# Kernel tuning notes

Measured on AMD Instinct MI355X. Metric: run time of the kernel, lower is better.

Reference implementation:

```python
import jax, jax.numpy as jnp
import numpy as np

B, N, DIM = 4, 4096, 1024
HEADS, DIM_HEAD = 16, 64
DIM_INNER = HEADS * DIM_HEAD
ATTN_SCALE = 8.0
EPS = 1e-12  # F.normalize default eps


def setup_inputs() -> dict:
    key = jax.random.key(0)
    k1, k2, k3, k4, k5 = jax.random.split(key, 5)
    x = jax.random.normal(k1, (B, N, DIM), dtype=jnp.float32)
    gamma = jnp.ones((DIM,), dtype=jnp.float32)
    # stored as (in, out) so forward is x @ w
    w_qkv = jax.random.normal(k2, (DIM, 3 * DIM_INNER), dtype=jnp.float32) * (DIM ** -0.5)
    temperature = jnp.ones((HEADS, 1, 1), dtype=jnp.float32)
    w_out = jax.random.normal(k3, (DIM_INNER, DIM), dtype=jnp.float32) * (DIM_INNER ** -0.5)
    return {"x": x, "gamma": gamma, "w_qkv": w_qkv, "temperature": temperature, "w_out": w_out}


def _l2norm(t):
    # F.normalize(t, dim=-1): t / max(||t||_2, eps)
    n = jnp.linalg.norm(t, axis=-1, keepdims=True)
    return t / jnp.maximum(n, EPS)


def reference(x, gamma, w_qkv, temperature, w_out):
    b, n, dim = x.shape
    # RMSNorm: F.normalize(x, dim=-1) * sqrt(dim) * gamma
    xn = _l2norm(x) * (dim ** 0.5) * gamma
    # QKV projection -> qkv b h d n
    qkv = (xn @ w_qkv).reshape(b, n, 3, HEADS, DIM_HEAD)
    qkv = qkv.transpose(2, 0, 3, 4, 1)  # (3, b, h, d, n)
    q, k, v = qkv[0], qkv[1], qkv[2]
    # l2-normalize q, k over the sequence (last) axis; temperature-scale q
    q = _l2norm(q) * jnp.exp(temperature)  # temperature: (h,1,1) broadcast
    k = _l2norm(k)
    # cross-covariance attention over the small channel dim d
    sim = jnp.einsum('bhdn,bhen->bhde', q, k) * ATTN_SCALE
    attn = jax.nn.softmax(sim, axis=-1)
    out = jnp.einsum('bhde,bhen->bhdn', attn, v)
    # b h d n -> b n (h d), then out projection
    out = out.transpose(0, 3, 1, 2).reshape(b, n, DIM_INNER)
    return out @ w_out
```

## Files before the change

kernel.cpp:

```cpp
#include <hip/hip_runtime.h>
#include <stdint.h>

typedef unsigned short u16;
typedef unsigned int u32;
typedef __attribute__((ext_vector_type(8))) __bf16 bf16x8;
typedef __attribute__((ext_vector_type(4))) float f32x4;

#define M_TOT 16384
#define DIMX  1024

__device__ __forceinline__ u16 f2b(float f) {
  u32 u = __builtin_bit_cast(u32, f);
  u32 r = (u + 0x7fffu + ((u >> 16) & 1u)) >> 16;
  return (u16)r;
}

__device__ __forceinline__ void gl2lds16(const void* g, void* l) {
  __builtin_amdgcn_global_load_lds((const __attribute__((address_space(1))) void*)g,
                                   (__attribute__((address_space(3))) void*)l,
                                   16, 0, 0);
}

__global__ __launch_bounds__(256) void k_rms(const float* __restrict__ x,
                                             const float* __restrict__ gamma,
                                             u16* __restrict__ xn) {
  int row = blockIdx.x;
  int t = threadIdx.x;
  const float4* xr = (const float4*)(x + (size_t)row * DIMX);
  float4 v = xr[t];
  float ss = v.x * v.x + v.y * v.y + v.z * v.z + v.w * v.w;
#pragma unroll
  for (int o = 32; o > 0; o >>= 1) ss += __shfl_xor(ss, o, 64);
  __shared__ float wss[4];
  int w = t >> 6;
  if ((t & 63) == 0) wss[w] = ss;
  __syncthreads();
  float tot = wss[0] + wss[1] + wss[2] + wss[3];
  float scale = 32.0f / fmaxf(sqrtf(tot), 1e-12f);
  float4 g = ((const float4*)gamma)[t];
  ushort4 o4;
  o4.x = f2b(v.x * scale * g.x);
  o4.y = f2b(v.y * scale * g.y);
  o4.z = f2b(v.z * scale * g.z);
  o4.w = f2b(v.w * scale * g.w);
  ((ushort4*)xn)[(size_t)row * 256 + t] = o4;
}

__global__ __launch_bounds__(256) void k_castT2(const float* __restrict__ wqkv,
                                                const float* __restrict__ wout,
                                                u16* __restrict__ wqT,
                                                u16* __restrict__ woT) {
  __shared__ float tile[32][33];
  const float* in; u16* out; int Cc; int c0;
  if (blockIdx.x < 96) { in = wqkv; out = wqT; Cc = 3072; c0 = blockIdx.x * 32; }
  else                 { in = wout; out = woT; Cc = 1024; c0 = (blockIdx.x - 96) * 32; }
  int r0 = blockIdx.y * 32;
  int tx = threadIdx.x, ty = threadIdx.y;
#pragma unroll
  for (int i = 0; i < 4; i++)
    tile[ty + i * 8][tx] = in[(size_t)(r0 + ty + i * 8) * Cc + c0 + tx];
  __syncthreads();
#pragma unroll
  for (int i = 0; i < 4; i++)
    out[(size_t)(c0 + ty + i * 8) * 1024 + r0 + tx] = f2b(tile[tx][ty + i * 8]);
}


template<bool SWAP>
__device__ __forceinline__ f32x4 mf(bf16x8 a, bf16x8 b, f32x4 c) {
  return SWAP ? __builtin_amdgcn_mfma_f32_16x16x32_bf16(b, a, c, 0, 0, 0)
              : __builtin_amdgcn_mfma_f32_16x16x32_bf16(a, b, c, 0, 0, 0);
}

__device__ __forceinline__ void stage_ab(const u16* __restrict__ Ag,
                                         const u16* __restrict__ Bg,
                                         u16* dstA, u16* dstB, int t, int k0) {
#pragma unroll
  for (int r = 0; r < 2; r++) {
    int c = r * 512 + t;
    int row = c >> 2, s = c & 3;
    int g = s ^ ((row >> 1) & 3);
    gl2lds16(Ag + (size_t)row * 1024 + k0 + g * 8,
             dstA + (r * 512 + (t >> 6) * 64) * 8);
  }
  {
    int row = t >> 2, s = t & 3;
    int g = s ^ ((row >> 1) & 3);
    gl2lds16(Bg + (size_t)row * 1024 + k0 + g * 8,
             dstB + ((t >> 6) * 64) * 8);
  }
}

template<bool SWAP>
__device__ __forceinline__ void gemm_core(const u16* __restrict__ Ag,
                                          const u16* __restrict__ Bg,
                                          u16* lds, int t, f32x4 (&acc)[4][4]) {
  const int lane = t & 63;
  const int r16 = lane & 15, q = lane >> 4;
  const int wr = (t >> 6) >> 1, wc = (t >> 6) & 1;
  const int arow = wr * 64 + r16;
  const int brow = wc * 64 + r16;

  stage_ab(Ag, Bg, lds, lds + 8192, t, 0);
  asm volatile("s_waitcnt vmcnt(0)" ::: "memory");
  __builtin_amdgcn_s_barrier();

  bf16x8 af[4], bf[4];
#pragma unroll 1
  for (int tt = 0; tt < 32; tt++) {
    const int cur = (tt & 1) ? 12288 : 0;
    const int nxt = cur ^ 12288;
    const int k1 = ((tt + 1) & 31) << 5;
    stage_ab(Ag, Bg, lds + nxt, lds + nxt + 8192, t, k1);
    const u16* A = lds + cur;
    const u16* B = lds + cur + 8192;
#pragma unroll
    for (int i = 0; i < 4; i++) {
      int ar = i * 16 + arow;
      int br = i * 16 + brow;
      af[i] = *(const bf16x8*)(A + ar * 32 + (q ^ ((ar >> 1) & 3)) * 8);
      bf[i] = *(const bf16x8*)(B + br * 32 + (q ^ ((br >> 1) & 3)) * 8);
    }
    __builtin_amdgcn_s_setprio(1);
#pragma unroll
    for (int i = 0; i < 4; i++)
#pragma unroll
      for (int j = 0; j < 4; j++)
        acc[i][j] = mf<SWAP>(af[i], bf[j], acc[i][j]);
    __builtin_amdgcn_s_setprio(0);
    asm volatile("s_waitcnt vmcnt(0)" ::: "memory");
    __builtin_amdgcn_s_barrier();
  }
}

__global__ __launch_bounds__(512, 4) void k_gemm1(const u16* __restrict__ A,
                                                  const u16* __restrict__ Bt,
                                                  u16* __restrict__ qkT,
                                                  u16* __restrict__ vmat,
                                                  float* __restrict__ sumsq) {
  __shared__ u16 lds[2 * 12288];
  int l = blockIdx.x;
  int xcd = l & 7, c = l >> 3;
  int mt = xcd * 8 + (c & 7);
  int nt = c >> 3;
  int m0 = mt * 256, n0 = nt * 128;
  int t = threadIdx.x, lane = t & 63;
  int r16 = lane & 15, q = lane >> 4;
  int wr = (t >> 6) >> 1, wc = (t >> 6) & 1;
  f32x4 acc[4][4] = {};
  if (n0 < 2048) {
    gemm_core<false>(A + (size_t)m0 * 1024, Bt + (size_t)n0 * 1024, lds, t, acc);
    int b = m0 >> 12;
#pragma unroll
    for (int j = 0; j < 4; j++) {
      int cc = n0 + wc * 64 + j * 16 + r16;
      float colss = 0.f;
#pragma unroll
      for (int i = 0; i < 4; i++) {
        f32x4 a = acc[i][j];
        colss += a.x * a.x + a.y * a.y + a.z * a.z + a.w * a.w;
        int m = m0 + wr * 64 + i * 16 + q * 4;
        ushort4 o4;
        o4.x = f2b(a.x); o4.y = f2b(a.y); o4.z = f2b(a.z); o4.w = f2b(a.w);
        *(ushort4*)(qkT + (size_t)cc * M_TOT + m) = o4;
      }
      colss += __shfl_xor(colss, 16, 64);
      colss += __shfl_xor(colss, 32, 64);
      if (lane < 16) atomicAdd(&sumsq[b * 2048 + cc], colss);
    }
  } else {
    gemm_core<true>(A + (size_t)m0 * 1024, Bt + (size_t)n0 * 1024, lds, t, acc);
    int vc0 = n0 - 2048;
#pragma unroll
    for (int i = 0; i < 4; i++) {
      int m = m0 + wr * 64 + i * 16 + r16;
#pragma unroll
      for (int j = 0; j < 4; j++) {
        int cc = vc0 + wc * 64 + j * 16 + q * 4;
        f32x4 a = acc[i][j];
        ushort4 o4;
        o4.x = f2b(a.x); o4.y = f2b(a.y); o4.z = f2b(a.z); o4.w = f2b(a.w);
        *(ushort4*)(vmat + (size_t)m * 1024 + cc) = o4;
      }
    }
  }
}

__global__ __launch_bounds__(256) void k_attn_s(const u16* __restrict__ qkT,
                                                float* __restrict__ Spart) {
  __shared__ u16 Ql[64 * 256];
  __shared__ u16 Kl[64 * 256];
  int bh = blockIdx.x, split = blockIdx.y;
  int b = bh >> 4, h = bh & 15;
  int t = threadIdx.x, lane = t & 63, w = t >> 6;
  int r16 = lane & 15, q = lane >> 4;
  const u16* qbase = qkT + (size_t)(h * 64) * M_TOT + b * 4096 + split * 1024;
  const u16* kbase = qkT + (size_t)(1024 + h * 64) * M_TOT + b * 4096 + split * 1024;
  int drow = w * 16 + r16;
  f32x4 acc[4] = {};
#pragma unroll 1
  for (int it = 0; it < 4; it++) {
    int ncol = it * 256;
#pragma unroll
    for (int r = 0; r < 8; r++) {
      int ch = r * 256 + t;
      int row = ch >> 5;
      int sl = (ch & 31) ^ (row & 31);
      gl2lds16(qbase + (size_t)row * M_TOT + ncol + sl * 8,
               Ql + (r * 256 + w * 64) * 8);
      gl2lds16(kbase + (size_t)row * M_TOT + ncol + sl * 8,
               Kl + (r * 256 + w * 64) * 8);
    }
    asm volatile("s_waitcnt vmcnt(0)" ::: "memory");
    __syncthreads();
#pragma unroll
    for (int it2 = 0; it2 < 8; it2++) {
      bf16x8 aq = *(const bf16x8*)(Ql + drow * 256 + (((it2 * 4 + q) ^ (drow & 31)) * 8));
#pragma unroll
      for (int j = 0; j < 4; j++) {
        int erow = j * 16 + r16;
        bf16x8 bk = *(const bf16x8*)(Kl + erow * 256 + (((it2 * 4 + q) ^ (erow & 31)) * 8));
        acc[j] = __builtin_amdgcn_mfma_f32_16x16x32_bf16(bk, aq, acc[j], 0, 0, 0);
      }
    }
    __syncthreads();
  }
  float* Sp = Spart + ((size_t)split * 64 + bh) * 4096;
#pragma unroll
  for (int j = 0; j < 4; j++)
    *(f32x4*)(Sp + drow * 64 + j * 16 + q * 4) = acc[j];
}

__global__ __launch_bounds__(256) void k_softmax(const float* __restrict__ Spart,
                                                 const float* __restrict__ sumsq,
                                                 const float* __restrict__ temp,
                                                 u16* __restrict__ PT) {
  int bh = blockIdx.x;
  int b = bh >> 4, h = bh & 15;
  int t = threadIdx.x;
  int d = t & 63, w = t >> 6;
  int e0 = w * 16;
  __shared__ float rnk[64];
  __shared__ float redm[4][64];
  __shared__ float reds[4][64];
  if (t < 64) rnk[t] = 1.0f / fmaxf(sqrtf(sumsq[b * 2048 + 1024 + h * 64 + t]), 1e-12f);
  __syncthreads();
  float nq = sqrtf(sumsq[b * 2048 + h * 64 + d]);
  float qs = 8.0f * __expf(temp[h]) / fmaxf(nq, 1e-12f);
  const float* Sp = Spart + (size_t)bh * 4096 + d * 64 + e0;
  float vals[16];
#pragma unroll
  for (int e = 0; e < 16; e += 4) {
    f32x4 v = {};
#pragma unroll
    for (int s = 0; s < 4; s++)
      v += *(const f32x4*)(Sp + (size_t)s * 64 * 4096 + e);
    vals[e + 0] = v.x; vals[e + 1] = v.y; vals[e + 2] = v.z; vals[e + 3] = v.w;
  }
  float mx = -3.0e38f;
#pragma unroll
  for (int e = 0; e < 16; e++) {
    float v = vals[e] * qs * rnk[e0 + e];
    vals[e] = v;
    mx = fmaxf(mx, v);
  }
  redm[w][d] = mx;
  __syncthreads();
  float M = fmaxf(fmaxf(redm[0][d], redm[1][d]), fmaxf(redm[2][d], redm[3][d]));
  float s = 0.f;
#pragma unroll
  for (int e = 0; e < 16; e++) {
    float v = __expf(vals[e] - M);
    vals[e] = v;
    s += v;
  }
  reds[w][d] = s;
  __syncthreads();
  float inv = 1.0f / (reds[0][d] + reds[1][d] + reds[2][d] + reds[3][d]);
#pragma unroll
  for (int e = 0; e < 16; e++)
    PT[((size_t)bh * 64 + e0 + e) * 64 + d] = f2b(vals[e] * inv);
}

__global__ __launch_bounds__(256) void k_m(const u16* __restrict__ woT,
                                           const u16* __restrict__ PT,
                                           u16* __restrict__ MT) {
  int bh = blockIdx.x;
  int b = bh >> 4, h = bh & 15;
  int o0 = blockIdx.y * 128;
  int t = threadIdx.x, lane = t & 63, w = t >> 6;
  int r16 = lane & 15, q = lane >> 4;
  const u16* pbase = PT + (size_t)bh * 4096;
  f32x4 acc[2][4] = {};
#pragma unroll
  for (int ks = 0; ks < 2; ks++) {
    int kk = ks * 32 + q * 8;
    bf16x8 af[2], bfr[4];
#pragma unroll
    for (int i = 0; i < 2; i++)
      af[i] = *(const bf16x8*)(woT + (size_t)(o0 + w * 32 + i * 16 + r16) * 1024 + h * 64 + kk);
#pragma unroll
    for (int j = 0; j < 4; j++)
      bfr[j] = *(const bf16x8*)(pbase + (size_t)(j * 16 + r16) * 64 + kk);
#pragma unroll
    for (int i = 0; i < 2; i++)
#pragma unroll
      for (int j = 0; j < 4; j++)
        acc[i][j] = __builtin_amdgcn_mfma_f32_16x16x32_bf16(af[i], bfr[j], acc[i][j], 0, 0, 0);
  }
  u16* dst = MT + (size_t)b * 1024 * 1024;
#pragma unroll
  for (int i = 0; i < 2; i++) {
    int o = o0 + w * 32 + i * 16 + q * 4;
#pragma unroll
    for (int j = 0; j < 4; j++) {
      int e = h * 64 + j * 16 + r16;
      f32x4 a = acc[i][j];
      dst[(size_t)(o + 0) * 1024 + e] = f2b(a.x);
      dst[(size_t)(o + 1) * 1024 + e] = f2b(a.y);
      dst[(size_t)(o + 2) * 1024 + e] = f2b(a.z);
      dst[(size_t)(o + 3) * 1024 + e] = f2b(a.w);
    }
  }
}

__global__ __launch_bounds__(512, 4) void k_gemm2(const u16* __restrict__ A,
                                                  const u16* __restrict__ Bt,
                                                  float* __restrict__ C) {
  __shared__ u16 lds[2 * 12288];
  int l = blockIdx.x;
  int xcd = l & 7, c = l >> 3;
  int mt = xcd * 8 + (c & 7);
  int nt = c >> 3;
  int m0 = mt * 256, n0 = nt * 128;
  int b = m0 >> 12;
  const u16* Bb = Bt + (size_t)b * 1024 * 1024;
  int t = threadIdx.x, lane = t & 63;
  int r16 = lane & 15, q = lane >> 4;
  int wr = (t >> 6) >> 1, wc = (t >> 6) & 1;
  f32x4 acc[4][4] = {};
  gemm_core<true>(A + (size_t)m0 * 1024, Bb + (size_t)n0 * 1024, lds, t, acc);
#pragma unroll
  for (int i = 0; i < 4; i++) {
    int m = m0 + wr * 64 + i * 16 + r16;
#pragma unroll
    for (int j = 0; j < 4; j++) {
      int cc = n0 + wc * 64 + j * 16 + q * 4;
      *(f32x4*)(C + (size_t)m * 1024 + cc) = acc[i][j];
    }
  }
}

extern "C" void kernel_launch(void* const* d_in, const int* in_sizes, int n_in,
                              void* d_out, int out_size, void* d_ws, size_t ws_size,
                              hipStream_t stream) {
  const float* x     = (const float*)d_in[0];
  const float* gamma = (const float*)d_in[1];
  const float* wqkv  = (const float*)d_in[2];
  const float* temp  = (const float*)d_in[3];
  const float* wout  = (const float*)d_in[4];
  float* out = (float*)d_out;

  char* ws = (char*)d_ws;
  size_t off = 0;
  u16* xn = (u16*)(ws + off);    off += (size_t)M_TOT * 1024 * 2;
  u16* wqT = (u16*)(ws + off);   off += (size_t)3072 * 1024 * 2;
  u16* woT = (u16*)(ws + off);   off += (size_t)1024 * 1024 * 2;
  u16* qkT = (u16*)(ws + off);   off += (size_t)2048 * M_TOT * 2;
  u16* vmat = (u16*)(ws + off);  off += (size_t)M_TOT * 1024 * 2;
  float* sumsq = (float*)(ws + off); off += (size_t)4 * 2048 * 4;
  u16* PT = (u16*)(ws + off);    off += (size_t)64 * 64 * 64 * 2;
  u16* MT = (u16*)(ws + off);    off += (size_t)4 * 1024 * 1024 * 2;

  float* Spart = (float*)xn;

  hipMemsetAsync((void*)sumsq, 0, (size_t)4 * 2048 * 4, stream);

  k_rms<<<16384, 256, 0, stream>>>(x, gamma, xn);
  dim3 cb(32, 8);
  k_castT2<<<dim3(128, 32), cb, 0, stream>>>(wqkv, wout, wqT, woT);
  k_gemm1<<<1536, 512, 0, stream>>>(xn, wqT, qkT, vmat, sumsq);
  k_attn_s<<<dim3(64, 4), 256, 0, stream>>>(qkT, Spart);
  k_softmax<<<64, 256, 0, stream>>>(Spart, sumsq, temp, PT);
  k_m<<<dim3(64, 8), 256, 0, stream>>>(woT, PT, MT);
  k_gemm2<<<512, 512, 0, stream>>>(vmat, MT, out);
}
```

Baseline: 326.3 us.

## Reassociate attention via per-batch Gram matrix of normalized inputs

Computes the per-batch Gram matrix G = xn^T xn (1024x1024) once and derives the q·k similarities and the q/k column norms from W_q^T G W_k, so the full QKV projection over all tokens is no longer materialised. The value and output projections are folded into one per-batch matrix (W_v · attn-derived M), and the final output is a single GEMM of xn with it. This replaces the large 16384x3072 projection with smaller 1024-sized GEMMs, at the cost of an extra transpose of xn, a split-K partial buffer, and more bf16 rounding of intermediate products.

```diff
diff --git a/kernel.cpp b/kernel.cpp
--- a/kernel.cpp
+++ b/kernel.cpp
@@ -49,20 +49,48 @@
 __global__ __launch_bounds__(256) void k_castT2(const float* __restrict__ wqkv,
                                                 const float* __restrict__ wout,
                                                 u16* __restrict__ wqT,
-                                                u16* __restrict__ woT) {
+                                                u16* __restrict__ woT,
+                                                u16* __restrict__ wvc) {
   __shared__ float tile[32][33];
-  const float* in; u16* out; int Cc; int c0;
-  if (blockIdx.x < 96) { in = wqkv; out = wqT; Cc = 3072; c0 = blockIdx.x * 32; }
-  else                 { in = wout; out = woT; Cc = 1024; c0 = (blockIdx.x - 96) * 32; }
+  int bx = blockIdx.x;
   int r0 = blockIdx.y * 32;
   int tx = threadIdx.x, ty = threadIdx.y;
-#pragma unroll
-  for (int i = 0; i < 4; i++)
-    tile[ty + i * 8][tx] = in[(size_t)(r0 + ty + i * 8) * Cc + c0 + tx];
+  if (bx < 96) {
+    const float* in; u16* out; int Cc; int c0;
+    if (bx < 64) { in = wqkv; out = wqT; Cc = 3072; c0 = bx * 32; }
+    else         { in = wout; out = woT; Cc = 1024; c0 = (bx - 64) * 32; }
+#pragma unroll
+    for (int i = 0; i < 4; i++)
+      tile[ty + i * 8][tx] = in[(size_t)(r0 + ty + i * 8) * Cc + c0 + tx];
+    __syncthreads();
+#pragma unroll
+    for (int i = 0; i < 4; i++)
+      out[(size_t)(c0 + ty + i * 8) * 1024 + r0 + tx] = f2b(tile[tx][ty + i * 8]);
+  } else {
+    int c0 = (bx - 96) * 32;
+#pragma unroll
+    for (int i = 0; i < 4; i++) {
+      int r = r0 + ty + i * 8;
+      wvc[(size_t)r * 1024 + c0 + tx] = f2b(wqkv[(size_t)r * 3072 + 2048 + c0 + tx]);
+    }
+  }
+}
+
+__global__ __launch_bounds__(256) void k_xT(const u16* __restrict__ xn,
+                                            u16* __restrict__ xnT) {
+  __shared__ u16 tile[64][65];
+  int bz = blockIdx.z;
+  int n0 = blockIdx.x * 64, c0 = blockIdx.y * 64;
+  int tx = threadIdx.x, ty = threadIdx.y;
+  const u16* in = xn + (size_t)bz * 4096 * 1024;
+  u16* out = xnT + (size_t)bz * 1024 * 4096;
+#pragma unroll
+  for (int i = 0; i < 16; i++)
+    tile[ty + i * 4][tx] = in[(size_t)(n0 + ty + i * 4) * 1024 + c0 + tx];
   __syncthreads();
 #pragma unroll
-  for (int i = 0; i < 4; i++)
-    out[(size_t)(c0 + ty + i * 8) * 1024 + r0 + tx] = f2b(tile[tx][ty + i * 8]);
+  for (int i = 0; i < 16; i++)
+    out[(size_t)(c0 + ty + i * 4) * 4096 + n0 + tx] = tile[tx][ty + i * 4];
 }
 
 
@@ -74,19 +102,20 @@
 
 __device__ __forceinline__ void stage_ab(const u16* __restrict__ Ag,
                                          const u16* __restrict__ Bg,
-                                         u16* dstA, u16* dstB, int t, int k0) {
+                                         u16* dstA, u16* dstB, int t, int k0,
+                                         int ldA, int ldB) {
 #pragma unroll
   for (int r = 0; r < 2; r++) {
     int c = r * 512 + t;
     int row = c >> 2, s = c & 3;
     int g = s ^ ((row >> 1) & 3);
-    gl2lds16(Ag + (size_t)row * 1024 + k0 + g * 8,
+    gl2lds16(Ag + (size_t)row * ldA + k0 + g * 8,
              dstA + (r * 512 + (t >> 6) * 64) * 8);
   }
   {
     int row = t >> 2, s = t & 3;
     int g = s ^ ((row >> 1) & 3);
-    gl2lds16(Bg + (size_t)row * 1024 + k0 + g * 8,
+    gl2lds16(Bg + (size_t)row * ldB + k0 + g * 8,
              dstB + ((t >> 6) * 64) * 8);
   }
 }
@@ -94,24 +123,25 @@
 template<bool SWAP>
 __device__ __forceinline__ void gemm_core(const u16* __restrict__ Ag,
                                           const u16* __restrict__ Bg,
-                                          u16* lds, int t, f32x4 (&acc)[4][4]) {
+                                          u16* lds, int t, f32x4 (&acc)[4][4],
+                                          int ldA, int ldB, int nsteps) {
   const int lane = t & 63;
   const int r16 = lane & 15, q = lane >> 4;
   const int wr = (t >> 6) >> 1, wc = (t >> 6) & 1;
   const int arow = wr * 64 + r16;
   const int brow = wc * 64 + r16;
 
-  stage_ab(Ag, Bg, lds, lds + 8192, t, 0);
+  stage_ab(Ag, Bg, lds, lds + 8192, t, 0, ldA, ldB);
   asm volatile("s_waitcnt vmcnt(0)" ::: "memory");
   __builtin_amdgcn_s_barrier();
 
   bf16x8 af[4], bf[4];
 #pragma unroll 1
-  for (int tt = 0; tt < 32; tt++) {
+  for (int tt = 0; tt < nsteps; tt++) {
     const int cur = (tt & 1) ? 12288 : 0;
     const int nxt = cur ^ 12288;
-    const int k1 = ((tt + 1) & 31) << 5;
-    stage_ab(Ag, Bg, lds + nxt, lds + nxt + 8192, t, k1);
+    int k1 = (tt + 1 == nsteps) ? 0 : (tt + 1) * 32;
+    stage_ab(Ag, Bg, lds + nxt, lds + nxt + 8192, t, k1, ldA, ldB);
     const u16* A = lds + cur;
     const u16* B = lds + cur + 8192;
 #pragma unroll
@@ -133,106 +163,120 @@
   }
 }
 
-__global__ __launch_bounds__(512, 4) void k_gemm1(const u16* __restrict__ A,
-                                                  const u16* __restrict__ Bt,
-                                                  u16* __restrict__ qkT,
-                                                  u16* __restrict__ vmat,
-                                                  float* __restrict__ sumsq) {
+__global__ __launch_bounds__(512, 4) void k_G(const u16* __restrict__ xnT,
+                                              float* __restrict__ Gp) {
   __shared__ u16 lds[2 * 12288];
   int l = blockIdx.x;
-  int xcd = l & 7, c = l >> 3;
-  int mt = xcd * 8 + (c & 7);
-  int nt = c >> 3;
+  int s = l & 3, b = (l >> 2) & 3;
+  int tile = l >> 4;
+  int mt = tile >> 3, nt = tile & 7;
+  int m0 = mt * 256, n0 = nt * 128;
+  const u16* base = xnT + (size_t)b * 1024 * 4096 + s * 1024;
+  int t = threadIdx.x, lane = t & 63;
+  int r16 = lane & 15, q = lane >> 4;
+  int wr = (t >> 6) >> 1, wc = (t >> 6) & 1;
+  f32x4 acc[4][4] = {};
+  gemm_core<true>(base + (size_t)m0 * 4096, base + (size_t)n0 * 4096,
+                  lds, t, acc, 4096, 4096, 32);
+  float* C = Gp + (size_t)(s * 4 + b) * 1048576;
+#pragma unroll
+  for (int i = 0; i < 4; i++) {
+    int m = m0 + wr * 64 + i * 16 + r16;
+#pragma unroll
+    for (int j = 0; j < 4; j++) {
+      int cc = n0 + wc * 64 + j * 16 + q * 4;
+      *(f32x4*)(C + (size_t)m * 1024 + cc) = acc[i][j];
+    }
+  }
+}
+
+__global__ __launch_bounds__(256) void k_Gred(const float* __restrict__ Gp,
+                                              u16* __restrict__ G) {
+  size_t i = ((size_t)blockIdx.x * 256 + threadIdx.x) * 4;
+  f32x4 v = {};
+#pragma unroll
+  for (int s = 0; s < 4; s++)
+    v += *(const f32x4*)(Gp + (size_t)s * 4194304 + i);
+  ushort4 o4;
+  o4.x = f2b(v.x); o4.y = f2b(v.y); o4.z = f2b(v.z); o4.w = f2b(v.w);
+  *(ushort4*)(G + i) = o4;
+}
+
+__global__ __launch_bounds__(512, 4) void k_V(const u16* __restrict__ wqT,
+                                              const u16* __restrict__ G,
+                                              u16* __restrict__ V) {
+  __shared__ u16 lds[2 * 12288];
+  int l = blockIdx.x;
+  int b = l & 3;
+  int tile = l >> 2;
+  int mt = tile >> 3, nt = tile & 7;
   int m0 = mt * 256, n0 = nt * 128;
   int t = threadIdx.x, lane = t & 63;
   int r16 = lane & 15, q = lane >> 4;
   int wr = (t >> 6) >> 1, wc = (t >> 6) & 1;
   f32x4 acc[4][4] = {};
-  if (n0 < 2048) {
-    gemm_core<false>(A + (size_t)m0 * 1024, Bt + (size_t)n0 * 1024, lds, t, acc);
-    int b = m0 >> 12;
+  gemm_core<true>(wqT + (size_t)m0 * 1024,
+                  G + (size_t)b * 1048576 + (size_t)n0 * 1024,
+                  lds, t, acc, 1024, 1024, 32);
+  u16* out = V + (size_t)b * 2097152;
+#pragma unroll
+  for (int i = 0; i < 4; i++) {
+    int m = m0 + wr * 64 + i * 16 + r16;
 #pragma unroll
     for (int j = 0; j < 4; j++) {
-      int cc = n0 + wc * 64 + j * 16 + r16;
-      float colss = 0.f;
-#pragma unroll
-      for (int i = 0; i < 4; i++) {
-        f32x4 a = acc[i][j];
-        colss += a.x * a.x + a.y * a.y + a.z * a.z + a.w * a.w;
-        int m = m0 + wr * 64 + i * 16 + q * 4;
-        ushort4 o4;
-        o4.x = f2b(a.x); o4.y = f2b(a.y); o4.z = f2b(a.z); o4.w = f2b(a.w);
-        *(ushort4*)(qkT + (size_t)cc * M_TOT + m) = o4;
-      }
-      colss += __shfl_xor(colss, 16, 64);
-      colss += __shfl_xor(colss, 32, 64);
-      if (lane < 16) atomicAdd(&sumsq[b * 2048 + cc], colss);
-    }
-  } else {
-    gemm_core<true>(A + (size_t)m0 * 1024, Bt + (size_t)n0 * 1024, lds, t, acc);
-    int vc0 = n0 - 2048;
-#pragma unroll
-    for (int i = 0; i < 4; i++) {
-      int m = m0 + wr * 64 + i * 16 + r16;
-#pragma unroll
-      for (int j = 0; j < 4; j++) {
-        int cc = vc0 + wc * 64 + j * 16 + q * 4;
-        f32x4 a = acc[i][j];
-        ushort4 o4;
-        o4.x = f2b(a.x); o4.y = f2b(a.y); o4.z = f2b(a.z); o4.w = f2b(a.w);
-        *(ushort4*)(vmat + (size_t)m * 1024 + cc) = o4;
-      }
-    }
-  }
-}
-
-__global__ __launch_bounds__(256) void k_attn_s(const u16* __restrict__ qkT,
-                                                float* __restrict__ Spart) {
-  __shared__ u16 Ql[64 * 256];
-  __shared__ u16 Kl[64 * 256];
-  int bh = blockIdx.x, split = blockIdx.y;
+      int cc = n0 + wc * 64 + j * 16 + q * 4;
+      f32x4 a = acc[i][j];
+      ushort4 o4;
+      o4.x = f2b(a.x); o4.y = f2b(a.y); o4.z = f2b(a.z); o4.w = f2b(a.w);
+      *(ushort4*)(out + (size_t)m * 1024 + cc) = o4;
+    }
+  }
+}
+
+__global__ __launch_bounds__(256) void k_S(const u16* __restrict__ V,
+                                           const u16* __restrict__ wqT,
+                                           float* __restrict__ Sbuf,
+                                           float* __restrict__ norms) {
+  int bh = blockIdx.x;
   int b = bh >> 4, h = bh & 15;
   int t = threadIdx.x, lane = t & 63, w = t >> 6;
   int r16 = lane & 15, q = lane >> 4;
-  const u16* qbase = qkT + (size_t)(h * 64) * M_TOT + b * 4096 + split * 1024;
-  const u16* kbase = qkT + (size_t)(1024 + h * 64) * M_TOT + b * 4096 + split * 1024;
+  const u16* Vb = V + (size_t)b * 2097152;
+  const u16* v2 = Vb + (size_t)(h * 64) * 1024;
+  const u16* wk = wqT + (size_t)(1024 + h * 64) * 1024;
   int drow = w * 16 + r16;
   f32x4 acc[4] = {};
-#pragma unroll 1
-  for (int it = 0; it < 4; it++) {
-    int ncol = it * 256;
-#pragma unroll
-    for (int r = 0; r < 8; r++) {
-      int ch = r * 256 + t;
-      int row = ch >> 5;
-      int sl = (ch & 31) ^ (row & 31);
-      gl2lds16(qbase + (size_t)row * M_TOT + ncol + sl * 8,
-               Ql + (r * 256 + w * 64) * 8);
-      gl2lds16(kbase + (size_t)row * M_TOT + ncol + sl * 8,
-               Kl + (r * 256 + w * 64) * 8);
-    }
-    asm volatile("s_waitcnt vmcnt(0)" ::: "memory");
-    __syncthreads();
-#pragma unroll
-    for (int it2 = 0; it2 < 8; it2++) {
-      bf16x8 aq = *(const bf16x8*)(Ql + drow * 256 + (((it2 * 4 + q) ^ (drow & 31)) * 8));
-#pragma unroll
-      for (int j = 0; j < 4; j++) {
-        int erow = j * 16 + r16;
-        bf16x8 bk = *(const bf16x8*)(Kl + erow * 256 + (((it2 * 4 + q) ^ (erow & 31)) * 8));
-        acc[j] = __builtin_amdgcn_mfma_f32_16x16x32_bf16(bk, aq, acc[j], 0, 0, 0);
-      }
-    }
-    __syncthreads();
-  }
-  float* Sp = Spart + ((size_t)split * 64 + bh) * 4096;
+#pragma unroll 4
+  for (int kk = 0; kk < 1024; kk += 32) {
+    bf16x8 aq = *(const bf16x8*)(v2 + (size_t)drow * 1024 + kk + q * 8);
+#pragma unroll
+    for (int j = 0; j < 4; j++) {
+      bf16x8 bk = *(const bf16x8*)(wk + (size_t)(j * 16 + r16) * 1024 + kk + q * 8);
+      acc[j] = __builtin_amdgcn_mfma_f32_16x16x32_bf16(bk, aq, acc[j], 0, 0, 0);
+    }
+  }
+  float* Sp = Sbuf + (size_t)bh * 4096;
 #pragma unroll
   for (int j = 0; j < 4; j++)
     *(f32x4*)(Sp + drow * 64 + j * 16 + q * 4) = acc[j];
-}
-
-__global__ __launch_bounds__(256) void k_softmax(const float* __restrict__ Spart,
-                                                 const float* __restrict__ sumsq,
+  if (t < 128) {
+    int row = (t < 64) ? (h * 64 + t) : (1024 + h * 64 + (t - 64));
+    const u16* vr = Vb + (size_t)row * 1024;
+    const u16* wr2 = wqT + (size_t)row * 1024;
+    float s = 0.f;
+#pragma unroll 4
+    for (int c = 0; c < 1024; c += 8) {
+      bf16x8 a = *(const bf16x8*)(vr + c);
+      bf16x8 bb = *(const bf16x8*)(wr2 + c);
+#pragma unroll
+      for (int k = 0; k < 8; k++) s += (float)a[k] * (float)bb[k];
+    }
+    norms[b * 2048 + row] = s;
+  }
+}
+
+__global__ __launch_bounds__(256) void k_softmax(const float* __restrict__ Sbuf,
+                                                 const float* __restrict__ norms,
                                                  const float* __restrict__ temp,
                                                  u16* __restrict__ PT) {
   int bh = blockIdx.x;
@@ -243,18 +287,15 @@
   __shared__ float rnk[64];
   __shared__ float redm[4][64];
   __shared__ float reds[4][64];
-  if (t < 64) rnk[t] = 1.0f / fmaxf(sqrtf(sumsq[b * 2048 + 1024 + h * 64 + t]), 1e-12f);
+  if (t < 64) rnk[t] = 1.0f / fmaxf(sqrtf(norms[b * 2048 + 1024 + h * 64 + t]), 1e-12f);
   __syncthreads();
-  float nq = sqrtf(sumsq[b * 2048 + h * 64 + d]);
+  float nq = sqrtf(norms[b * 2048 + h * 64 + d]);
   float qs = 8.0f * __expf(temp[h]) / fmaxf(nq, 1e-12f);
-  const float* Sp = Spart + (size_t)bh * 4096 + d * 64 + e0;
+  const float* Sp = Sbuf + (size_t)bh * 4096 + d * 64 + e0;
   float vals[16];
 #pragma unroll
   for (int e = 0; e < 16; e += 4) {
-    f32x4 v = {};
-#pragma unroll
-    for (int s = 0; s < 4; s++)
-      v += *(const f32x4*)(Sp + (size_t)s * 64 * 4096 + e);
+    f32x4 v = *(const f32x4*)(Sp + e);
     vals[e + 0] = v.x; vals[e + 1] = v.y; vals[e + 2] = v.z; vals[e + 3] = v.w;
   }
   float mx = -3.0e38f;
@@ -324,8 +365,39 @@
   }
 }
 
-__global__ __launch_bounds__(512, 4) void k_gemm2(const u16* __restrict__ A,
-                                                  const u16* __restrict__ Bt,
+__global__ __launch_bounds__(512, 4) void k_M2(const u16* __restrict__ wvc,
+                                               const u16* __restrict__ MT,
+                                               u16* __restrict__ Mt) {
+  __shared__ u16 lds[2 * 12288];
+  int l = blockIdx.x;
+  int b = l & 3;
+  int tile = l >> 2;
+  int mt = tile >> 3, nt = tile & 7;
+  int m0 = mt * 256, n0 = nt * 128;
+  int t = threadIdx.x, lane = t & 63;
+  int r16 = lane & 15, q = lane >> 4;
+  int wr = (t >> 6) >> 1, wc = (t >> 6) & 1;
+  f32x4 acc[4][4] = {};
+  gemm_core<false>(wvc + (size_t)m0 * 1024,
+                   MT + (size_t)b * 1048576 + (size_t)n0 * 1024,
+                   lds, t, acc, 1024, 1024, 32);
+  u16* out = Mt + (size_t)b * 1048576;
+#pragma unroll
+  for (int j = 0; j < 4; j++) {
+    int cc = n0 + wc * 64 + j * 16 + r16;
+#pragma unroll
+    for (int i = 0; i < 4; i++) {
+      int m = m0 + wr * 64 + i * 16 + q * 4;
+      f32x4 a = acc[i][j];
+      ushort4 o4;
+      o4.x = f2b(a.x); o4.y = f2b(a.y); o4.z = f2b(a.z); o4.w = f2b(a.w);
+      *(ushort4*)(out + (size_t)cc * 1024 + m) = o4;
+    }
+  }
+}
+
+__global__ __launch_bounds__(512, 4) void k_final(const u16* __restrict__ xn,
+                                                  const u16* __restrict__ Mt,
                                                   float* __restrict__ C) {
   __shared__ u16 lds[2 * 12288];
   int l = blockIdx.x;
@@ -334,12 +406,13 @@
   int nt = c >> 3;
   int m0 = mt * 256, n0 = nt * 128;
   int b = m0 >> 12;
-  const u16* Bb = Bt + (size_t)b * 1024 * 1024;
   int t = threadIdx.x, lane = t & 63;
   int r16 = lane & 15, q = lane >> 4;
   int wr = (t >> 6) >> 1, wc = (t >> 6) & 1;
   f32x4 acc[4][4] = {};
-  gemm_core<true>(A + (size_t)m0 * 1024, Bb + (size_t)n0 * 1024, lds, t, acc);
+  gemm_core<true>(xn + (size_t)m0 * 1024,
+                  Mt + (size_t)b * 1048576 + (size_t)n0 * 1024,
+                  lds, t, acc, 1024, 1024, 32);
 #pragma unroll
   for (int i = 0; i < 4; i++) {
     int m = m0 + wr * 64 + i * 16 + r16;
@@ -362,26 +435,30 @@
   float* out = (float*)d_out;
 
   char* ws = (char*)d_ws;
-  size_t off = 0;
-  u16* xn = (u16*)(ws + off);    off += (size_t)M_TOT * 1024 * 2;
-  u16* wqT = (u16*)(ws + off);   off += (size_t)3072 * 1024 * 2;
-  u16* woT = (u16*)(ws + off);   off += (size_t)1024 * 1024 * 2;
-  u16* qkT = (u16*)(ws + off);   off += (size_t)2048 * M_TOT * 2;
-  u16* vmat = (u16*)(ws + off);  off += (size_t)M_TOT * 1024 * 2;
-  float* sumsq = (float*)(ws + off); off += (size_t)4 * 2048 * 4;
-  u16* PT = (u16*)(ws + off);    off += (size_t)64 * 64 * 64 * 2;
-  u16* MT = (u16*)(ws + off);    off += (size_t)4 * 1024 * 1024 * 2;
-
-  float* Spart = (float*)xn;
-
-  hipMemsetAsync((void*)sumsq, 0, (size_t)4 * 2048 * 4, stream);
+  u16* xn    = (u16*)(ws);
+  u16* xnT   = (u16*)(ws + 33554432);
+  u16* wqT   = (u16*)(ws + 67108864);
+  u16* woT   = (u16*)(ws + 71303168);
+  u16* wvc   = (u16*)(ws + 73400320);
+  u16* G     = (u16*)(ws + 75497472);
+  float* norms = (float*)(ws + 83886080);
+  char* R    = ws + 83918848;
+  float* Gp  = (float*)R;
+  u16* V     = (u16*)R;
+  float* Sbuf = (float*)(R + 16777216);
+  u16* PT    = (u16*)(R + 17825792);
+  u16* MT    = (u16*)(R + 18350080);
+  u16* Mt    = (u16*)(R + 26738688);
 
   k_rms<<<16384, 256, 0, stream>>>(x, gamma, xn);
-  dim3 cb(32, 8);
-  k_castT2<<<dim3(128, 32), cb, 0, stream>>>(wqkv, wout, wqT, woT);
-  k_gemm1<<<1536, 512, 0, stream>>>(xn, wqT, qkT, vmat, sumsq);
-  k_attn_s<<<dim3(64, 4), 256, 0, stream>>>(qkT, Spart);
-  k_softmax<<<64, 256, 0, stream>>>(Spart, sumsq, temp, PT);
+  k_castT2<<<dim3(128, 32), dim3(32, 8), 0, stream>>>(wqkv, wout, wqT, woT, wvc);
+  k_xT<<<dim3(64, 16, 4), dim3(64, 4), 0, stream>>>(xn, xnT);
+  k_G<<<512, 512, 0, stream>>>(xnT, Gp);
+  k_Gred<<<4096, 256, 0, stream>>>(Gp, G);
+  k_V<<<256, 512, 0, stream>>>(wqT, G, V);
+  k_S<<<64, 256, 0, stream>>>(V, wqT, Sbuf, norms);
+  k_softmax<<<64, 256, 0, stream>>>(Sbuf, norms, temp, PT);
   k_m<<<dim3(64, 8), 256, 0, stream>>>(woT, PT, MT);
-  k_gemm2<<<512, 512, 0, stream>>>(vmat, MT, out);
-}
+  k_M2<<<128, 512, 0, stream>>>(wvc, MT, Mt);
+  k_final<<<512, 512, 0, stream>>>(xn, Mt, out);
+}
```

Result: slower. 343.0 us (+5.1%).

## Merge RMSNorm and weight-cast kernels; retile output GEMM to 128x128 with K=64 stages

Applied to the files above, without the earlier changes.

The RMSNorm kernel and the weight transpose/cast kernel are fused into one launch, with the block index selecting the role. This removes one kernel launch and lets the two independent jobs overlap. The final output GEMM moves from 256x128 tiles with 512 threads and K=32 stages to 128x128 tiles with 256 threads and K=64 double-buffered stages using a new XOR swizzle. That doubles the grid to 1024 blocks for better CU occupancy and halves the number of barriers per K, at the cost of more redundant loads of B.

```diff
diff --git a/kernel.cpp b/kernel.cpp
--- a/kernel.cpp
+++ b/kernel.cpp
@@ -21,50 +21,53 @@
                                    16, 0, 0);
 }
 
-__global__ __launch_bounds__(256) void k_rms(const float* __restrict__ x,
+__global__ __launch_bounds__(256) void k_pre(const float* __restrict__ x,
                                              const float* __restrict__ gamma,
-                                             u16* __restrict__ xn) {
-  int row = blockIdx.x;
+                                             u16* __restrict__ xn,
+                                             const float* __restrict__ wqkv,
+                                             const float* __restrict__ wout,
+                                             u16* __restrict__ wqT,
+                                             u16* __restrict__ woT) {
+  __shared__ float tile[32][33];
+  int blk = blockIdx.x;
   int t = threadIdx.x;
-  const float4* xr = (const float4*)(x + (size_t)row * DIMX);
-  float4 v = xr[t];
-  float ss = v.x * v.x + v.y * v.y + v.z * v.z + v.w * v.w;
-#pragma unroll
-  for (int o = 32; o > 0; o >>= 1) ss += __shfl_xor(ss, o, 64);
-  __shared__ float wss[4];
-  int w = t >> 6;
-  if ((t & 63) == 0) wss[w] = ss;
-  __syncthreads();
-  float tot = wss[0] + wss[1] + wss[2] + wss[3];
-  float scale = 32.0f / fmaxf(sqrtf(tot), 1e-12f);
-  float4 g = ((const float4*)gamma)[t];
-  ushort4 o4;
-  o4.x = f2b(v.x * scale * g.x);
-  o4.y = f2b(v.y * scale * g.y);
-  o4.z = f2b(v.z * scale * g.z);
-  o4.w = f2b(v.w * scale * g.w);
-  ((ushort4*)xn)[(size_t)row * 256 + t] = o4;
-}
-
-__global__ __launch_bounds__(256) void k_castT2(const float* __restrict__ wqkv,
-                                                const float* __restrict__ wout,
-                                                u16* __restrict__ wqT,
-                                                u16* __restrict__ woT) {
-  __shared__ float tile[32][33];
-  const float* in; u16* out; int Cc; int c0;
-  if (blockIdx.x < 96) { in = wqkv; out = wqT; Cc = 3072; c0 = blockIdx.x * 32; }
-  else                 { in = wout; out = woT; Cc = 1024; c0 = (blockIdx.x - 96) * 32; }
-  int r0 = blockIdx.y * 32;
-  int tx = threadIdx.x, ty = threadIdx.y;
-#pragma unroll
-  for (int i = 0; i < 4; i++)
-    tile[ty + i * 8][tx] = in[(size_t)(r0 + ty + i * 8) * Cc + c0 + tx];
-  __syncthreads();
-#pragma unroll
-  for (int i = 0; i < 4; i++)
-    out[(size_t)(c0 + ty + i * 8) * 1024 + r0 + tx] = f2b(tile[tx][ty + i * 8]);
-}
-
+  if (blk < 16384) {
+    int row = blk;
+    const float4* xr = (const float4*)(x + (size_t)row * DIMX);
+    float4 v = xr[t];
+    float ss = v.x * v.x + v.y * v.y + v.z * v.z + v.w * v.w;
+#pragma unroll
+    for (int o = 32; o > 0; o >>= 1) ss += __shfl_xor(ss, o, 64);
+    float* wss = &tile[0][0];
+    int w = t >> 6;
+    if ((t & 63) == 0) wss[w] = ss;
+    __syncthreads();
+    float tot = wss[0] + wss[1] + wss[2] + wss[3];
+    float scale = 32.0f / fmaxf(sqrtf(tot), 1e-12f);
+    float4 g = ((const float4*)gamma)[t];
+    ushort4 o4;
+    o4.x = f2b(v.x * scale * g.x);
+    o4.y = f2b(v.y * scale * g.y);
+    o4.z = f2b(v.z * scale * g.z);
+    o4.w = f2b(v.w * scale * g.w);
+    ((ushort4*)xn)[(size_t)row * 256 + t] = o4;
+  } else {
+    int bb = blk - 16384;
+    int bx = bb & 127, by = bb >> 7;
+    int r0 = by * 32;
+    int tx = t & 31, ty = t >> 5;
+    const float* in; u16* out; int Cc; int c0;
+    if (bx < 96) { in = wqkv; out = wqT; Cc = 3072; c0 = bx * 32; }
+    else         { in = wout; out = woT; Cc = 1024; c0 = (bx - 96) * 32; }
+#pragma unroll
+    for (int i = 0; i < 4; i++)
+      tile[ty + i * 8][tx] = in[(size_t)(r0 + ty + i * 8) * Cc + c0 + tx];
+    __syncthreads();
+#pragma unroll
+    for (int i = 0; i < 4; i++)
+      out[(size_t)(c0 + ty + i * 8) * 1024 + r0 + tx] = f2b(tile[tx][ty + i * 8]);
+  }
+}
 
 template<bool SWAP>
 __device__ __forceinline__ f32x4 mf(bf16x8 a, bf16x8 b, f32x4 c) {
@@ -127,6 +130,65 @@
 #pragma unroll
       for (int j = 0; j < 4; j++)
         acc[i][j] = mf<SWAP>(af[i], bf[j], acc[i][j]);
+    __builtin_amdgcn_s_setprio(0);
+    asm volatile("s_waitcnt vmcnt(0)" ::: "memory");
+    __builtin_amdgcn_s_barrier();
+  }
+}
+
+__device__ __forceinline__ void stage128(const u16* __restrict__ g,
+                                         u16* dst, int t, int k0) {
+#pragma unroll
+  for (int r = 0; r < 4; r++) {
+    int c = r * 256 + t;
+    int row = c >> 3;
+    int sl = (c & 7) ^ (row & 7);
+    gl2lds16(g + (size_t)row * 1024 + k0 + sl * 8,
+             dst + (r * 256 + (t >> 6) * 64) * 8);
+  }
+}
+
+template<bool SWAP>
+__device__ __forceinline__ void gemm_core128(const u16* __restrict__ Ag,
+                                             const u16* __restrict__ Bg,
+                                             u16* lds, int t, f32x4 (&acc)[4][4]) {
+  const int lane = t & 63;
+  const int r16 = lane & 15, q = lane >> 4;
+  const int s0 = (q ^ (r16 & 7)) * 8;
+  const int wr = (t >> 6) >> 1, wc = (t >> 6) & 1;
+  const int arow = wr * 64 + r16;
+  const int brow = wc * 64 + r16;
+
+  stage128(Ag, lds + 0,    t, 0);
+  stage128(Bg, lds + 8192, t, 0);
+  asm volatile("s_waitcnt vmcnt(0)" ::: "memory");
+  __builtin_amdgcn_s_barrier();
+
+  bf16x8 af[4][2], bf[4][2];
+#pragma unroll 1
+  for (int tt = 0; tt < 16; tt++) {
+    const int bo = (tt & 1) << 14;
+    const int nb = bo ^ 16384;
+    const int k1 = ((tt + 1) & 15) << 6;
+    stage128(Ag, lds + nb,        t, k1);
+    stage128(Bg, lds + nb + 8192, t, k1);
+    const u16* A = lds + bo;
+    const u16* B = lds + bo + 8192;
+#pragma unroll
+    for (int i = 0; i < 4; i++) {
+      af[i][0] = *(const bf16x8*)(A + (i * 16 + arow) * 64 + s0);
+      af[i][1] = *(const bf16x8*)(A + (i * 16 + arow) * 64 + (s0 ^ 32));
+      bf[i][0] = *(const bf16x8*)(B + (i * 16 + brow) * 64 + s0);
+      bf[i][1] = *(const bf16x8*)(B + (i * 16 + brow) * 64 + (s0 ^ 32));
+    }
+    __builtin_amdgcn_s_setprio(1);
+#pragma unroll
+    for (int kq = 0; kq < 2; kq++)
+#pragma unroll
+      for (int i = 0; i < 4; i++)
+#pragma unroll
+        for (int j = 0; j < 4; j++)
+          acc[i][j] = mf<SWAP>(af[i][kq], bf[j][kq], acc[i][j]);
     __builtin_amdgcn_s_setprio(0);
     asm volatile("s_waitcnt vmcnt(0)" ::: "memory");
     __builtin_amdgcn_s_barrier();
@@ -324,22 +386,22 @@
   }
 }
 
-__global__ __launch_bounds__(512, 4) void k_gemm2(const u16* __restrict__ A,
+__global__ __launch_bounds__(256, 2) void k_gemm2(const u16* __restrict__ A,
                                                   const u16* __restrict__ Bt,
                                                   float* __restrict__ C) {
-  __shared__ u16 lds[2 * 12288];
+  __shared__ u16 lds[2 * 16384];
   int l = blockIdx.x;
   int xcd = l & 7, c = l >> 3;
-  int mt = xcd * 8 + (c & 7);
-  int nt = c >> 3;
-  int m0 = mt * 256, n0 = nt * 128;
+  int mt = xcd * 16 + (c & 15);
+  int nt = c >> 4;
+  int m0 = mt * 128, n0 = nt * 128;
   int b = m0 >> 12;
   const u16* Bb = Bt + (size_t)b * 1024 * 1024;
   int t = threadIdx.x, lane = t & 63;
   int r16 = lane & 15, q = lane >> 4;
   int wr = (t >> 6) >> 1, wc = (t >> 6) & 1;
   f32x4 acc[4][4] = {};
-  gemm_core<true>(A + (size_t)m0 * 1024, Bb + (size_t)n0 * 1024, lds, t, acc);
+  gemm_core128<true>(A + (size_t)m0 * 1024, Bb + (size_t)n0 * 1024, lds, t, acc);
 #pragma unroll
   for (int i = 0; i < 4; i++) {
     int m = m0 + wr * 64 + i * 16 + r16;
@@ -376,12 +438,10 @@
 
   hipMemsetAsync((void*)sumsq, 0, (size_t)4 * 2048 * 4, stream);
 
-  k_rms<<<16384, 256, 0, stream>>>(x, gamma, xn);
-  dim3 cb(32, 8);
-  k_castT2<<<dim3(128, 32), cb, 0, stream>>>(wqkv, wout, wqT, woT);
+  k_pre<<<16384 + 4096, 256, 0, stream>>>(x, gamma, xn, wqkv, wout, wqT, woT);
   k_gemm1<<<1536, 512, 0, stream>>>(xn, wqT, qkT, vmat, sumsq);
   k_attn_s<<<dim3(64, 4), 256, 0, stream>>>(qkT, Spart);
   k_softmax<<<64, 256, 0, stream>>>(Spart, sumsq, temp, PT);
   k_m<<<dim3(64, 8), 256, 0, stream>>>(woT, PT, MT);
-  k_gemm2<<<512, 512, 0, stream>>>(vmat, MT, out);
-}
+  k_gemm2<<<1024, 256, 0, stream>>>(vmat, MT, out);
+}
```

Measured after the change: 331.5 us. No clear change (+1.6%).
